# Optimization experiments

Measured on AMD Instinct MI355X. Metric: run time of the kernel, lower is better.

The kernel has to match this reference:

```python
import jax, jax.numpy as jnp
import numpy as np

NUM_EMBEDDINGS = 8192
EMBEDDING_DIM = 256
COMMITMENT_COST = 0.25


def setup_inputs() -> dict:
    key = jax.random.key(0)
    kz, ke = jax.random.split(key)
    z = jax.random.normal(kz, (16, 1024, EMBEDDING_DIM), dtype=jnp.float32)
    # nn.init.normal_(std=1/sqrt(embedding_dim))
    embedding = jax.random.normal(ke, (NUM_EMBEDDINGS, EMBEDDING_DIM), dtype=jnp.float32) / (EMBEDDING_DIM ** 0.5)
    return {"z": z, "embedding": embedding}


def reference(z, embedding):
    b, f, d = z.shape
    flat_z = z.reshape(-1, d)  # (N, d)
    # squared L2 distances to each codebook entry: (N, K)
    distances = (jnp.sum(flat_z * flat_z, axis=1, keepdims=True)
                 - 2.0 * flat_z @ embedding.T
                 + jnp.sum(embedding * embedding, axis=1))
    indices = jnp.argmin(distances, axis=1)  # (N,)
    z_q = embedding[indices].reshape(b, f, d)
    commitment_loss = jnp.mean((jax.lax.stop_gradient(z_q) - z) ** 2)
    vq_loss = commitment_loss * COMMITMENT_COST
    z_q_st = z + jax.lax.stop_gradient(z_q - z)  # straight-through
    return z_q_st, indices.reshape(b, f), vq_loss
```

## Files before the change

### kernel.cpp

```cpp
#include <hip/hip_runtime.h>
#include <math.h>

#define D_DIM   256
#define N_ROWS  16384
#define K_CODES 8192
#define NCHUNK  8

typedef __attribute__((ext_vector_type(8))) _Float16 h8v;
typedef __attribute__((ext_vector_type(4))) float f4v;
typedef __attribute__((ext_vector_type(4))) unsigned short us4;
typedef unsigned long long u64;
typedef unsigned int u32;

#define IDX_OFF  ((size_t)N_ROWS * D_DIM)
#define LOSS_OFF (IDX_OFF + N_ROWS)

#define WS_ENORM_OFF    (2u * 1024u * 1024u)
#define WS_PARTIAL_OFF  (WS_ENORM_OFF + 32768u)
#define WS_ZH_OFF       (3u * 1024u * 1024u)
#define WS_EH_OFF       (11u * 1024u * 1024u)

__device__ __forceinline__ unsigned short f2h(float f) {
    _Float16 h = (_Float16)f;
    unsigned short u;
    __builtin_memcpy(&u, &h, 2);
    return u;
}
__device__ __forceinline__ u32 f2ord(float f) {
    u32 u = __float_as_uint(f);
    return (u & 0x80000000u) ? ~u : (u | 0x80000000u);
}
__device__ __forceinline__ void gl2lds16(const void* g, void* l) {
    __builtin_amdgcn_global_load_lds(
        (const __attribute__((address_space(1))) unsigned int*)g,
        (__attribute__((address_space(3))) unsigned int*)l, 16, 0, 0);
}

__global__ __launch_bounds__(256) void zconv_kernel(const float* __restrict__ z,
                                                    unsigned short* __restrict__ zh) {
    int q = blockIdx.x * 256 + threadIdx.x;
    float4 v = reinterpret_cast<const float4*>(z)[q];
    us4 h;
    h[0] = f2h(v.x); h[1] = f2h(v.y); h[2] = f2h(v.z); h[3] = f2h(v.w);
    int row = q >> 6;
    int f   = q & 63;
    int d0b = f >> 3, lg = (f >> 1) & 3, half = f & 1;
    size_t off = ((size_t)(d0b * 4 + lg) * N_ROWS + row) * 16 + half * 8;
    *reinterpret_cast<us4*>((char*)zh + off) = h;
}

__global__ __launch_bounds__(256) void econv_kernel(const float* __restrict__ emb,
                                                    unsigned short* __restrict__ eh,
                                                    float* __restrict__ enorm) {
    int q = blockIdx.x * 256 + threadIdx.x;
    float4 v = reinterpret_cast<const float4*>(emb)[q];

    float s = v.x * v.x + v.y * v.y + v.z * v.z + v.w * v.w;
    #pragma unroll
    for (int off = 32; off >= 1; off >>= 1) s += __shfl_down(s, off);

    us4 h;
    h[0] = f2h(v.x); h[1] = f2h(v.y); h[2] = f2h(v.z); h[3] = f2h(v.w);
    int row = q >> 6;
    int f   = q & 63;
    if (f == 0) enorm[row] = s;
    int d0b = f >> 3, lg = (f >> 1) & 3, half = f & 1;
    size_t off = ((size_t)(d0b * 4 + lg) * K_CODES + row) * 16 + half * 8;
    *reinterpret_cast<us4*>((char*)eh + off) = h;
}

__global__ __launch_bounds__(256, 3) void argmin_kernel(const unsigned short* __restrict__ zh,
                                                        const unsigned short* __restrict__ eh,
                                                        const float* __restrict__ enorm,
                                                        u64* __restrict__ cand) {
    __shared__ __align__(16) unsigned char lds[36864];

    const int tid = threadIdx.x;
    const int wv  = tid >> 6;
    const int l   = tid & 63;
    const int lr  = l & 15;
    const int lg  = l >> 4;
    const int wm  = wv >> 1;
    const int wn  = wv & 1;
    const int wg  = blockIdx.x;
    const int x   = wg & 7;
    const int i   = wg >> 3;
    const int ch  = i >> 4;
    const int r0    = x * 2048 + (i & 15) * 128;
    const int cbase = ch * 1024;

    const char* zhp = (const char*)zh;
    const char* ehp = (const char*)eh;

    {
        float4 ev = *reinterpret_cast<const float4*>(enorm + cbase + tid * 4);
        *reinterpret_cast<float4*>(lds + 32768 + tid * 16) = ev;
    }

    const int tsw = tid >> 7, tix = tid & 127;
    const size_t E0a = ((size_t)tsw       * K_CODES + cbase + tix) * 16;
    const size_t E0b = ((size_t)(tsw + 2) * K_CODES + cbase + tix) * 16;

    auto stage = [&](int s, int b) {
        char* dst = (char*)lds + b * 16384 + tid * 16;
        const size_t u0 = (((size_t)((s & 3) * 2)) << 19) + (((size_t)(s >> 2)) << 11);
        const size_t u1 = u0 + (1u << 19);
        gl2lds16(ehp + E0a + u0, dst);
        gl2lds16(ehp + E0b + u0, dst + 4096);
        gl2lds16(ehp + E0a + u1, dst + 8192);
        gl2lds16(ehp + E0b + u1, dst + 12288);
    };

    size_t Zb[4];
    #pragma unroll
    for (int j = 0; j < 4; ++j)
        Zb[j] = ((size_t)lg * N_ROWS + r0 + wm * 64 + j * 16 + lr) * 16;

    u64 t1[4], t2[4];
    #pragma unroll
    for (int j = 0; j < 4; ++j) { t1[j] = ~0ULL; t2[j] = ~0ULL; }

    f4v acc[4][4];
    #pragma unroll
    for (int i2 = 0; i2 < 4; ++i2)
        #pragma unroll
        for (int j = 0; j < 4; ++j)
            acc[i2][j] = (f4v){0.f, 0.f, 0.f, 0.f};

    stage(0, 0);
    __syncthreads();

    for (int s = 0; s < 32; ++s) {
        const int b = s & 1;
        if (s + 1 < 32) stage(s + 1, b ^ 1);

        h8v zCur[2][4];
        {
            const int dd = (s & 3) * 2;
            #pragma unroll
            for (int h = 0; h < 2; ++h)
                #pragma unroll
                for (int j = 0; j < 4; ++j)
                    zCur[h][j] = *reinterpret_cast<const h8v*>(
                        zhp + Zb[j] + ((size_t)(dd + h) << 20));
        }
        {
            const char* base = (const char*)lds + b * 16384;
            #pragma unroll
            for (int h = 0; h < 2; ++h)
                #pragma unroll
                for (int i2 = 0; i2 < 4; ++i2) {
                    int code = wn * 64 + i2 * 16 + lr;
                    h8v ehf = *reinterpret_cast<const h8v*>(
                        base + h * 8192 + lg * 2048 + code * 16);
                    #pragma unroll
                    for (int j = 0; j < 4; ++j)
                        acc[i2][j] = __builtin_amdgcn_mfma_f32_16x16x32_f16(
                            ehf, zCur[h][j], acc[i2][j], 0, 0, 0);
                }
        }

        if ((s & 3) == 3) {
            const int cbl = (s >> 2) * 128;
            const int cb  = cbase + cbl;
            float en[16];
            #pragma unroll
            for (int i2 = 0; i2 < 4; ++i2)
                #pragma unroll
                for (int r = 0; r < 4; ++r)
                    en[i2 * 4 + r] = *reinterpret_cast<const float*>(
                        lds + 32768 + (cbl + wn * 64 + i2 * 16 + lg * 4 + r) * 4);
            #pragma unroll
            for (int j = 0; j < 4; ++j) {
                float v1[8], v2[8]; int g1[8], g2[8];
                #pragma unroll
                for (int k = 0; k < 8; ++k) {
                    int a = 2 * k, c = 2 * k + 1;
                    float da = fmaf(-2.f, acc[a >> 2][j][a & 3], en[a]);
                    float dc = fmaf(-2.f, acc[c >> 2][j][c & 3], en[c]);
                    bool w = dc < da;
                    v1[k] = w ? dc : da; g1[k] = w ? c : a;
                    v2[k] = w ? da : dc; g2[k] = w ? a : c;
                }
                #pragma unroll
                for (int st = 4; st >= 1; st >>= 1)
                    #pragma unroll
                    for (int m = 0; m < st; ++m) {
                        float b1 = v1[m + st], b2 = v2[m + st];
                        int  b1s = g1[m + st], b2s = g2[m + st];
                        bool c1 = b1 < v1[m];
                        float hv = c1 ? v1[m] : b1;  int hs = c1 ? g1[m] : b1s;
                        v1[m] = c1 ? b1 : v1[m];     g1[m] = c1 ? b1s : g1[m];
                        bool c2 = b2 < v2[m];
                        float mv = c2 ? b2 : v2[m];  int ms = c2 ? b2s : g2[m];
                        bool c3 = mv < hv;
                        v2[m] = c3 ? mv : hv;        g2[m] = c3 ? ms : hs;
                    }
                int s1 = g1[0], s2 = g2[0];
                u32 code1 = (u32)(cb + wn * 64 + ((s1 >> 2) << 4) + lg * 4 + (s1 & 3));
                u32 code2 = (u32)(cb + wn * 64 + ((s2 >> 2) << 4) + lg * 4 + (s2 & 3));
                u64 k1 = ((u64)f2ord(v1[0]) << 32) | code1;
                u64 k2 = ((u64)f2ord(v2[0]) << 32) | code2;
                u64 n1 = k1 < t1[j] ? k1 : t1[j];
                u64 hi = k1 < t1[j] ? t1[j] : k1;
                u64 m2 = k2 < t2[j] ? k2 : t2[j];
                t1[j] = n1;
                t2[j] = hi < m2 ? hi : m2;
            }
            #pragma unroll
            for (int i2 = 0; i2 < 4; ++i2)
                #pragma unroll
                for (int j = 0; j < 4; ++j)
                    acc[i2][j] = (f4v){0.f, 0.f, 0.f, 0.f};
        }

        __syncthreads();
    }

    #pragma unroll
    for (int j = 0; j < 4; ++j) {
        u64 a1 = t1[j], a2 = t2[j];
        #pragma unroll
        for (int mk = 16; mk <= 32; mk <<= 1) {
            u64 o1 = __shfl_xor(a1, mk);
            u64 o2 = __shfl_xor(a2, mk);
            u64 n1 = a1 < o1 ? a1 : o1;
            u64 hi = a1 < o1 ? o1 : a1;
            u64 m2 = a2 < o2 ? a2 : o2;
            a1 = n1;
            a2 = hi < m2 ? hi : m2;
        }
        t1[j] = a1; t2[j] = a2;
    }

    __syncthreads();
    u64* mbuf = (u64*)lds;
    if (wn == 1 && lg == 0) {
        #pragma unroll
        for (int j = 0; j < 4; ++j) {
            int s = ((wm * 4 + j) * 16 + lr) * 2;
            mbuf[s] = t1[j]; mbuf[s + 1] = t2[j];
        }
    }
    __syncthreads();
    if (wn == 0 && lg == 0) {
        #pragma unroll
        for (int j = 0; j < 4; ++j) {
            int s = ((wm * 4 + j) * 16 + lr) * 2;
            u64 b1 = mbuf[s], b2 = mbuf[s + 1];
            u64 n1 = t1[j] < b1 ? t1[j] : b1;
            u64 hi = t1[j] < b1 ? b1 : t1[j];
            u64 m2 = t2[j] < b2 ? t2[j] : b2;
            u64 n2 = hi < m2 ? hi : m2;
            int row = r0 + wm * 64 + j * 16 + lr;
            cand[((size_t)row * NCHUNK + ch) * 2]     = n1;
            cand[((size_t)row * NCHUNK + ch) * 2 + 1] = n2;
        }
    }
}

__global__ __launch_bounds__(256) void rescore_kernel(const float* __restrict__ z,
                                                      const float* __restrict__ emb,
                                                      const float* __restrict__ enorm,
                                                      const u64* __restrict__ cand,
                                                      float* __restrict__ out,
                                                      float* __restrict__ partials) {
    int row  = blockIdx.x * 4 + (threadIdx.x >> 6);
    int lane = threadIdx.x & 63;
    float4 zv = reinterpret_cast<const float4*>(z)[(size_t)row * 64 + lane];

    u64 best = ~0ULL;
    for (int s = 0; s < 2 * NCHUNK; ++s) {
        u32 c = ((u32)cand[(size_t)row * (2 * NCHUNK) + s]) & (K_CODES - 1);
        float4 ev = reinterpret_cast<const float4*>(emb)[(size_t)c * 64 + lane];
        float p = zv.x * ev.x + zv.y * ev.y + zv.z * ev.z + zv.w * ev.w;
        #pragma unroll
        for (int mk = 1; mk < 64; mk <<= 1) p += __shfl_xor(p, mk);
        float dist = fmaf(-2.f, p, enorm[c]);
        u64 key = ((u64)f2ord(dist) << 32) | c;
        best = key < best ? key : best;
    }
    u32 idx = ((u32)best) & (K_CODES - 1);
    if (lane == 0) out[IDX_OFF + row] = (float)idx;

    float4 ev = reinterpret_cast<const float4*>(emb)[(size_t)idx * 64 + lane];
    float tx = ev.x - zv.x, ty = ev.y - zv.y, tz = ev.z - zv.z, tw = ev.w - zv.w;
    float4 o;
    o.x = zv.x + tx; o.y = zv.y + ty; o.z = zv.z + tz; o.w = zv.w + tw;
    reinterpret_cast<float4*>(out)[(size_t)row * 64 + lane] = o;

    float s = tx * tx + ty * ty + tz * tz + tw * tw;
    #pragma unroll
    for (int off = 32; off >= 1; off >>= 1) s += __shfl_down(s, off);

    __shared__ float wsum[4];
    if (lane == 0) wsum[threadIdx.x >> 6] = s;
    __syncthreads();
    if (threadIdx.x == 0)
        partials[blockIdx.x] = (wsum[0] + wsum[1]) + (wsum[2] + wsum[3]);
}

__global__ __launch_bounds__(256) void loss_kernel(const float* __restrict__ partials,
                                                   float* __restrict__ out) {
    __shared__ float sm[256];
    float s = 0.0f;
    for (int i = threadIdx.x; i < 4096; i += 256) s += partials[i];
    sm[threadIdx.x] = s;
    __syncthreads();
    #pragma unroll
    for (int st = 128; st >= 1; st >>= 1) {
        if (threadIdx.x < st) sm[threadIdx.x] += sm[threadIdx.x + st];
        __syncthreads();
    }
    if (threadIdx.x == 0)
        out[LOSS_OFF] = sm[0] * (0.25f / (float)(N_ROWS * D_DIM));
}

extern "C" void kernel_launch(void* const* d_in, const int* in_sizes, int n_in,
                              void* d_out, int out_size, void* d_ws, size_t ws_size,
                              hipStream_t stream) {
    const float* z   = (const float*)d_in[0];
    const float* emb = (const float*)d_in[1];
    float* out = (float*)d_out;

    u64*   cand     = (u64*)d_ws;
    float* enorm    = (float*)((char*)d_ws + WS_ENORM_OFF);
    float* partials = (float*)((char*)d_ws + WS_PARTIAL_OFF);
    unsigned short* zh = (unsigned short*)((char*)d_ws + WS_ZH_OFF);
    unsigned short* eh = (unsigned short*)((char*)d_ws + WS_EH_OFF);

    zconv_kernel<<<4096, 256, 0, stream>>>(z, zh);
    econv_kernel<<<2048, 256, 0, stream>>>(emb, eh, enorm);
    argmin_kernel<<<1024, 256, 0, stream>>>(zh, eh, enorm, cand);
    rescore_kernel<<<N_ROWS / 4, 256, 0, stream>>>(z, emb, enorm, cand, out, partials);
    loss_kernel<<<1, 256, 0, stream>>>(partials, out);
}
```

Baseline: 146.4 us.

## Keep the full z tile in registers across codebook tiles in argmin kernel

After: 135.6 us (median of 2 runs). -7.4%, faster.

```diff
diff --git a/kernel.cpp b/kernel.cpp
--- a/kernel.cpp
+++ b/kernel.cpp
@@ -69,7 +69,7 @@
     *reinterpret_cast<us4*>((char*)eh + off) = h;
 }
 
-__global__ __launch_bounds__(256, 3) void argmin_kernel(const unsigned short* __restrict__ zh,
+__global__ __launch_bounds__(256, 2) void argmin_kernel(const unsigned short* __restrict__ zh,
                                                         const unsigned short* __restrict__ eh,
                                                         const float* __restrict__ enorm,
                                                         u64* __restrict__ cand) {
@@ -101,9 +101,9 @@
     const size_t E0a = ((size_t)tsw       * K_CODES + cbase + tix) * 16;
     const size_t E0b = ((size_t)(tsw + 2) * K_CODES + cbase + tix) * 16;
 
-    auto stage = [&](int s, int b) {
+    auto stage2 = [&](int ctn, int qq, int b) {
         char* dst = (char*)lds + b * 16384 + tid * 16;
-        const size_t u0 = (((size_t)((s & 3) * 2)) << 19) + (((size_t)(s >> 2)) << 11);
+        const size_t u0 = (((size_t)(qq * 2)) << 19) + (((size_t)ctn) << 11);
         const size_t u1 = u0 + (1u << 19);
         gl2lds16(ehp + E0a + u0, dst);
         gl2lds16(ehp + E0b + u0, dst + 4096);
@@ -111,10 +111,19 @@
         gl2lds16(ehp + E0b + u1, dst + 12288);
     };
 
-    size_t Zb[4];
-    #pragma unroll
-    for (int j = 0; j < 4; ++j)
-        Zb[j] = ((size_t)lg * N_ROWS + r0 + wm * 64 + j * 16 + lr) * 16;
+    h8v zAll[8][4];
+    {
+        size_t Zb[4];
+        #pragma unroll
+        for (int j = 0; j < 4; ++j)
+            Zb[j] = ((size_t)lg * N_ROWS + r0 + wm * 64 + j * 16 + lr) * 16;
+        #pragma unroll
+        for (int d = 0; d < 8; ++d)
+            #pragma unroll
+            for (int j = 0; j < 4; ++j)
+                zAll[d][j] = *reinterpret_cast<const h8v*>(
+                    zhp + Zb[j] + ((size_t)d << 20));
+    }
 
     u64 t1[4], t2[4];
     #pragma unroll
@@ -127,94 +136,88 @@
         for (int j = 0; j < 4; ++j)
             acc[i2][j] = (f4v){0.f, 0.f, 0.f, 0.f};
 
-    stage(0, 0);
-    __syncthreads();
-
-    for (int s = 0; s < 32; ++s) {
-        const int b = s & 1;
-        if (s + 1 < 32) stage(s + 1, b ^ 1);
-
-        h8v zCur[2][4];
-        {
-            const int dd = (s & 3) * 2;
-            #pragma unroll
-            for (int h = 0; h < 2; ++h)
+    stage2(0, 0, 0);
+    __syncthreads();
+
+    for (int ct = 0; ct < 8; ++ct) {
+        #pragma unroll
+        for (int q = 0; q < 4; ++q) {
+            const int b = q & 1;
+            if (q < 3)           stage2(ct, q + 1, b ^ 1);
+            else if (ct < 7)     stage2(ct + 1, 0, 0);
+
+            {
+                const char* base = (const char*)lds + b * 16384;
                 #pragma unroll
-                for (int j = 0; j < 4; ++j)
-                    zCur[h][j] = *reinterpret_cast<const h8v*>(
-                        zhp + Zb[j] + ((size_t)(dd + h) << 20));
-        }
-        {
-            const char* base = (const char*)lds + b * 16384;
-            #pragma unroll
-            for (int h = 0; h < 2; ++h)
+                for (int h = 0; h < 2; ++h)
+                    #pragma unroll
+                    for (int i2 = 0; i2 < 4; ++i2) {
+                        int code = wn * 64 + i2 * 16 + lr;
+                        h8v ehf = *reinterpret_cast<const h8v*>(
+                            base + h * 8192 + lg * 2048 + code * 16);
+                        #pragma unroll
+                        for (int j = 0; j < 4; ++j)
+                            acc[i2][j] = __builtin_amdgcn_mfma_f32_16x16x32_f16(
+                                ehf, zAll[2 * q + h][j], acc[i2][j], 0, 0, 0);
+                    }
+            }
+
+            if (q == 3) {
+                const int cbl = ct * 128;
+                const int cb  = cbase + cbl;
+                float en[16];
                 #pragma unroll
-                for (int i2 = 0; i2 < 4; ++i2) {
-                    int code = wn * 64 + i2 * 16 + lr;
-                    h8v ehf = *reinterpret_cast<const h8v*>(
-                        base + h * 8192 + lg * 2048 + code * 16);
-                    #pragma unroll
-                    for (int j = 0; j < 4; ++j)
-                        acc[i2][j] = __builtin_amdgcn_mfma_f32_16x16x32_f16(
-                            ehf, zCur[h][j], acc[i2][j], 0, 0, 0);
-                }
-        }
-
-        if ((s & 3) == 3) {
-            const int cbl = (s >> 2) * 128;
-            const int cb  = cbase + cbl;
-            float en[16];
-            #pragma unroll
-            for (int i2 = 0; i2 < 4; ++i2)
+                for (int i2 = 0; i2 < 4; ++i2)
+                    #pragma unroll
+                    for (int r = 0; r < 4; ++r)
+                        en[i2 * 4 + r] = *reinterpret_cast<const float*>(
+                            lds + 32768 + (cbl + wn * 64 + i2 * 16 + lg * 4 + r) * 4);
                 #pragma unroll
-                for (int r = 0; r < 4; ++r)
-                    en[i2 * 4 + r] = *reinterpret_cast<const float*>(
-                        lds + 32768 + (cbl + wn * 64 + i2 * 16 + lg * 4 + r) * 4);
-            #pragma unroll
-            for (int j = 0; j < 4; ++j) {
-                float v1[8], v2[8]; int g1[8], g2[8];
-                #pragma unroll
-                for (int k = 0; k < 8; ++k) {
-                    int a = 2 * k, c = 2 * k + 1;
-                    float da = fmaf(-2.f, acc[a >> 2][j][a & 3], en[a]);
-                    float dc = fmaf(-2.f, acc[c >> 2][j][c & 3], en[c]);
-                    bool w = dc < da;
-                    v1[k] = w ? dc : da; g1[k] = w ? c : a;
-                    v2[k] = w ? da : dc; g2[k] = w ? a : c;
+                for (int j = 0; j < 4; ++j) {
+                    float v1[8], v2[8]; int g1[8], g2[8];
+                    #pragma unroll
+                    for (int k = 0; k < 8; ++k) {
+                        int a = 2 * k, c = 2 * k + 1;
+                        float da = fmaf(-2.f, acc[a >> 2][j][a & 3], en[a]);
+                        float dc = fmaf(-2.f, acc[c >> 2][j][c & 3], en[c]);
+                        bool w = dc < da;
+                        v1[k] = w ? dc : da; g1[k] = w ? c : a;
+                        v2[k] = w ? da : dc; g2[k] = w ? a : c;
+                    }
+                    #pragma unroll
+                    for (int st = 4; st >= 1; st >>= 1)
+                        #pragma unroll
+                        for (int m = 0; m < st; ++m) {
+                            float b1 = v1[m + st], b2 = v2[m + st];
+                            int  b1s = g1[m + st], b2s = g2[m + st];
+                            bool c1 = b1 < v1[m];
+                            float hv = c1 ? v1[m] : b1;  int hs = c1 ? g1[m] : b1s;
+                            v1[m] = c1 ? b1 : v1[m];     g1[m] = c1 ? b1s : g1[m];
+                            bool c2 = b2 < v2[m];
+                            float mv = c2 ? b2 : v2[m];  int ms = c2 ? b2s : g2[m];
+                            bool c3 = mv < hv;
+                            v2[m] = c3 ? mv : hv;        g2[m] = c3 ? ms : hs;
+                        }
+                    int s1 = g1[0], s2 = g2[0];
+                    u32 code1 = (u32)(cb + wn * 64 + ((s1 >> 2) << 4) + lg * 4 + (s1 & 3));
+                    u32 code2 = (u32)(cb + wn * 64 + ((s2 >> 2) << 4) + lg * 4 + (s2 & 3));
+                    u64 k1 = ((u64)f2ord(v1[0]) << 32) | code1;
+                    u64 k2 = ((u64)f2ord(v2[0]) << 32) | code2;
+                    u64 n1 = k1 < t1[j] ? k1 : t1[j];
+                    u64 hi = k1 < t1[j] ? t1[j] : k1;
+                    u64 m2 = k2 < t2[j] ? k2 : t2[j];
+                    t1[j] = n1;
+                    t2[j] = hi < m2 ? hi : m2;
                 }
                 #pragma unroll
-                for (int st = 4; st >= 1; st >>= 1)
-                    #pragma unroll
-                    for (int m = 0; m < st; ++m) {
-                        float b1 = v1[m + st], b2 = v2[m + st];
-                        int  b1s = g1[m + st], b2s = g2[m + st];
-                        bool c1 = b1 < v1[m];
-                        float hv = c1 ? v1[m] : b1;  int hs = c1 ? g1[m] : b1s;
-                        v1[m] = c1 ? b1 : v1[m];     g1[m] = c1 ? b1s : g1[m];
-                        bool c2 = b2 < v2[m];
-                        float mv = c2 ? b2 : v2[m];  int ms = c2 ? b2s : g2[m];
-                        bool c3 = mv < hv;
-                        v2[m] = c3 ? mv : hv;        g2[m] = c3 ? ms : hs;
-                    }
-                int s1 = g1[0], s2 = g2[0];
-                u32 code1 = (u32)(cb + wn * 64 + ((s1 >> 2) << 4) + lg * 4 + (s1 & 3));
-                u32 code2 = (u32)(cb + wn * 64 + ((s2 >> 2) << 4) + lg * 4 + (s2 & 3));
-                u64 k1 = ((u64)f2ord(v1[0]) << 32) | code1;
-                u64 k2 = ((u64)f2ord(v2[0]) << 32) | code2;
-                u64 n1 = k1 < t1[j] ? k1 : t1[j];
-                u64 hi = k1 < t1[j] ? t1[j] : k1;
-                u64 m2 = k2 < t2[j] ? k2 : t2[j];
-                t1[j] = n1;
-                t2[j] = hi < m2 ? hi : m2;
+                for (int i2 = 0; i2 < 4; ++i2)
+                    #pragma unroll
+                    for (int j = 0; j < 4; ++j)
+                        acc[i2][j] = (f4v){0.f, 0.f, 0.f, 0.f};
             }
-            #pragma unroll
-            for (int i2 = 0; i2 < 4; ++i2)
-                #pragma unroll
-                for (int j = 0; j < 4; ++j)
-                    acc[i2][j] = (f4v){0.f, 0.f, 0.f, 0.f};
+
+            __syncthreads();
         }
-
-        __syncthreads();
     }
 
     #pragma unroll
```
